# Optimization experiments

Hardware: AMD Instinct MI355X
Metric: run time of the kernel (lower is better)

The kernel has to match this reference:

```python
import jax, jax.numpy as jnp
import numpy as np

D_MODEL = 768
NUM_HEADS = 12
DEPTH = D_MODEL // NUM_HEADS
LN_EPS = 1e-5


def setup_inputs() -> dict:
    key = jax.random.key(0)
    ks = jax.random.split(key, 5)
    B, S = 2, 2048
    scale = 1.0 / np.sqrt(D_MODEL)
    return {
        "Q": jax.random.normal(ks[0], (B, S, D_MODEL), jnp.float32),
        "W_q": jax.random.normal(ks[1], (D_MODEL, D_MODEL), jnp.float32) * scale,
        "b_q": jnp.zeros((D_MODEL,), jnp.float32),
        "W_k": jax.random.normal(ks[2], (D_MODEL, D_MODEL), jnp.float32) * scale,
        "b_k": jnp.zeros((D_MODEL,), jnp.float32),
        "W_v": jax.random.normal(ks[3], (D_MODEL, D_MODEL), jnp.float32) * scale,
        "b_v": jnp.zeros((D_MODEL,), jnp.float32),
        "W_o": jax.random.normal(ks[4], (D_MODEL, D_MODEL), jnp.float32) * scale,
        "b_o": jnp.zeros((D_MODEL,), jnp.float32),
        "ln_gamma": jnp.ones((D_MODEL,), jnp.float32),
        "ln_beta": jnp.zeros((D_MODEL,), jnp.float32),
    }


def _split_heads(x, B):
    # [B, S, D] -> [B, H, S, depth]
    return x.reshape(B, -1, NUM_HEADS, DEPTH).transpose(0, 2, 1, 3)


def reference(Q, W_q, b_q, W_k, b_k, W_v, b_v, W_o, b_o, ln_gamma, ln_beta):
    B = Q.shape[0]
    residual = Q
    # torch Linear: x @ W.T + b
    q = _split_heads(Q @ W_q.T + b_q, B)  # [B,H,S,dh]
    k = _split_heads(Q @ W_k.T + b_k, B)
    v = _split_heads(Q @ W_v.T + b_v, B)
    scores = jnp.einsum("bhqd,bhkd->bhqk", q, k) / jnp.sqrt(jnp.float32(DEPTH))
    attn = jax.nn.softmax(scores, axis=-1)
    out = jnp.einsum("bhqk,bhkd->bhqd", attn, v)
    out = out.transpose(0, 2, 1, 3).reshape(B, -1, D_MODEL)
    out = out @ W_o.T + b_o
    x = out + residual
    mu = jnp.mean(x, axis=-1, keepdims=True)
    var = jnp.mean(jnp.square(x - mu), axis=-1, keepdims=True)
    return (x - mu) * jax.lax.rsqrt(var + LN_EPS) * ln_gamma + ln_beta
```

## Files before the change

kernel.cpp:

```cpp
#include <hip/hip_runtime.h>
#include <hip/hip_bf16.h>

#define D_MODEL 768
#define S_LEN   2048
#define BATCH   2
#define NHEAD   12
#define DH      64
#define NTOK    (BATCH * S_LEN)

typedef __attribute__((ext_vector_type(8))) short bf16x8;
typedef __attribute__((ext_vector_type(4))) float f32x4;

__device__ inline unsigned short f2bf(float f) {
    union { float f; unsigned u; } v; v.f = f;
    unsigned u = v.u;
    u += 0x7fffu + ((u >> 16) & 1u);
    return (unsigned short)(u >> 16);
}

__device__ inline unsigned pack_bf2(float a, float b) {
    union { __hip_bfloat162 h2; unsigned u; } cv;
    cv.h2 = __float22bfloat162_rn(make_float2(a, b));
    return cv.u;
}

__device__ inline void stage16(const void* g, void* l) {
    __builtin_amdgcn_global_load_lds(
        (const __attribute__((address_space(1))) unsigned*)g,
        (__attribute__((address_space(3))) unsigned*)l, 16, 0, 0);
}

__global__ __launch_bounds__(256) void convert_kernel(
    const float* __restrict__ Q,
    const float* __restrict__ Wq, const float* __restrict__ Wk,
    const float* __restrict__ Wv, const float* __restrict__ Wo,
    unsigned short* __restrict__ Xb,
    unsigned short* __restrict__ Wqb, unsigned short* __restrict__ Wkb,
    unsigned short* __restrict__ Wvb, unsigned short* __restrict__ Wob)
{
    const int XV = NTOK * D_MODEL / 4;
    const int WV = D_MODEL * D_MODEL / 4;
    int idx = blockIdx.x * 256 + threadIdx.x;
    if (idx >= XV + 4 * WV) return;

    const float* src; unsigned short* dst; int off;
    if (idx < XV) { src = Q; dst = Xb; off = idx; }
    else {
        int i2 = idx - XV;
        int seg = i2 / WV; off = i2 - seg * WV;
        if      (seg == 0) { src = Wq; dst = Wqb; }
        else if (seg == 1) { src = Wk; dst = Wkb; }
        else if (seg == 2) { src = Wv; dst = Wvb; }
        else               { src = Wo; dst = Wob; }
    }
    float4 v = reinterpret_cast<const float4*>(src)[off];
    uint2 o;
    o.x = pack_bf2(v.x, v.y);
    o.y = pack_bf2(v.z, v.w);
    reinterpret_cast<uint2*>(dst)[off] = o;
}

#define STAGE_TILE(glob, rowstrideB, row0, k0, ldsbase, nIss)                 \
    _Pragma("unroll")                                                          \
    for (int i = 0; i < (nIss); ++i) {                                         \
        int L = i * 4096 + wv * 1024 + lane * 16;                              \
        int row = L >> 7;                                                      \
        int colb = (L & 127) ^ ((row & 7) << 4);                               \
        stage16((const char*)(glob) + (size_t)((row0) + row) * (rowstrideB)    \
                    + ((k0) << 1) + colb,                                      \
                (char*)(ldsbase) + i * 4096 + wv * 1024);                      \
    }

__global__ __launch_bounds__(256) void qkv_gemm_kernel(
    const unsigned short* __restrict__ Xb,
    const unsigned short* __restrict__ Wall,
    const float* __restrict__ bq, const float* __restrict__ bk,
    const float* __restrict__ bv,
    unsigned short* __restrict__ qb, unsigned short* __restrict__ kb,
    unsigned short* __restrict__ vtb)
{
    const int lane = threadIdx.x & 63;
    const int wv   = threadIdx.x >> 6;
    const int lr   = lane & 15;
    const int lg   = lane >> 4;
    const int row0g = blockIdx.y * 128;
    const int col0g = blockIdx.x * 64;

    __shared__ __align__(16) unsigned short At[2][128 * 64];
    __shared__ __align__(16) unsigned short Bt[2][64 * 64];

    f32x4 acc[2][4] = {};

    STAGE_TILE(Xb,   1536, row0g, 0, At[0], 4);
    STAGE_TILE(Wall, 1536, col0g, 0, Bt[0], 2);
    __syncthreads();

    for (int s = 0; s < 12; ++s) {
        int cur = s & 1;
        if (s < 11) {
            STAGE_TILE(Xb,   1536, row0g, (s + 1) * 64, At[cur ^ 1], 4);
            STAGE_TILE(Wall, 1536, col0g, (s + 1) * 64, Bt[cur ^ 1], 2);
        }
        bf16x8 a[2][2], b[4][2];
#pragma unroll
        for (int m = 0; m < 2; ++m) {
            int row = wv * 32 + m * 16 + lr, sw = (row & 7) << 4;
#pragma unroll
            for (int ks = 0; ks < 2; ++ks)
                a[m][ks] = *reinterpret_cast<const bf16x8*>(
                    (const char*)At[cur] + row * 128 + ((ks * 64 + lg * 16) ^ sw));
        }
#pragma unroll
        for (int n = 0; n < 4; ++n) {
            int row = n * 16 + lr, sw = (row & 7) << 4;
#pragma unroll
            for (int ks = 0; ks < 2; ++ks)
                b[n][ks] = *reinterpret_cast<const bf16x8*>(
                    (const char*)Bt[cur] + row * 128 + ((ks * 64 + lg * 16) ^ sw));
        }
#pragma unroll
        for (int ks = 0; ks < 2; ++ks)
#pragma unroll
            for (int m = 0; m < 2; ++m)
#pragma unroll
                for (int n = 0; n < 4; ++n)
                    acc[m][n] = __builtin_amdgcn_mfma_f32_16x16x32_bf16(
                        a[m][ks], b[n][ks], acc[m][n], 0, 0, 0);
        __syncthreads();
    }

    const int which   = blockIdx.x / 12;
    const int colbase = (blockIdx.x % 12) * 64;
    const float* bias = (which == 0) ? bq : (which == 1) ? bk : bv;
#pragma unroll
    for (int m = 0; m < 2; ++m) {
#pragma unroll
        for (int n = 0; n < 4; ++n) {
            int col = colbase + n * 16 + lr;
            float bval = bias[col];
            int h = col >> 6, d = col & 63;
            int rowg = row0g + wv * 32 + m * 16 + lg * 4;
            int bb = rowg >> 11, s0 = rowg & 2047;
            if (which == 2) {
                uint2 w;
                w.x = pack_bf2(acc[m][n][0] + bval, acc[m][n][1] + bval);
                w.y = pack_bf2(acc[m][n][2] + bval, acc[m][n][3] + bval);
                *reinterpret_cast<uint2*>(
                    vtb + ((size_t)(bb * NHEAD + h) * DH + d) * S_LEN + s0) = w;
            } else {
                unsigned short* dst = (which == 0) ? qb : kb;
#pragma unroll
                for (int r = 0; r < 4; ++r)
                    dst[((size_t)(bb * NHEAD + h) * S_LEN + s0 + r) * DH + d] =
                        f2bf(acc[m][n][r] + bval);
            }
        }
    }
}

#define ATTN_CHUNK(P, CI)                                                      \
    {                                                                          \
        if ((CI) < 31) {                                                       \
            stage16(kg0, sdK[(P) ^ 1]);                                        \
            stage16(kg1, sdK[(P) ^ 1] + 4096);                                 \
            stage16(vg0, sdV[(P) ^ 1]);                                        \
            stage16(vg1, sdV[(P) ^ 1] + 4096);                                 \
            kg0 += 8192; kg1 += 8192; vg0 += 128; vg1 += 128;                  \
        }                                                                      \
        f32x4 s[4] = {};                                                       \
        __builtin_amdgcn_s_setprio(1);                                         \
        _Pragma("unroll")                                                      \
        for (int kt = 0; kt < 4; ++kt) {                                       \
            bf16x8 ak0 = *(const bf16x8*)(rdK[P] + kt * 2048);                 \
            bf16x8 ak1 = *(const bf16x8*)(rdK[P] + kt * 2048 + oD);            \
            s[kt] = __builtin_amdgcn_mfma_f32_16x16x32_bf16(ak0, bq0, s[kt], 0, 0, 0); \
            s[kt] = __builtin_amdgcn_mfma_f32_16x16x32_bf16(ak1, bq1, s[kt], 0, 0, 0); \
        }                                                                      \
        __builtin_amdgcn_s_setprio(0);                                         \
        bf16x8 av0[4], av1[4];                                                 \
        _Pragma("unroll")                                                      \
        for (int t = 0; t < 4; ++t) {                                          \
            av0[t] = *(const bf16x8*)(rdV[P] + t * 2048);                      \
            av1[t] = *(const bf16x8*)(rdV[P] + t * 2048 + oD);                 \
        }                                                                      \
        float mxr = fmaxf(fmaxf(fmaxf(s[0][0], s[0][1]), fmaxf(s[0][2], s[0][3])), \
                          fmaxf(fmaxf(s[1][0], s[1][1]), fmaxf(s[1][2], s[1][3]))); \
        mxr = fmaxf(mxr, fmaxf(fmaxf(fmaxf(s[2][0], s[2][1]), fmaxf(s[2][2], s[2][3])), \
                               fmaxf(fmaxf(s[3][0], s[3][1]), fmaxf(s[3][2], s[3][3])))); \
        mxr = fmaxf(mxr, __shfl_xor(mxr, 16));                                 \
        mxr = fmaxf(mxr, __shfl_xor(mxr, 32));                                 \
        float mxs = mxr * SC;                                                  \
        if (__any(mxs > m + 8.0f)) {                                           \
            float mn = fmaxf(m, mxs);                                          \
            float sf = __builtin_amdgcn_exp2f(m - mn);                         \
            m = mn; l *= sf;                                                   \
            _Pragma("unroll")                                                  \
            for (int t = 0; t < 4; ++t) acc[t] *= sf;                          \
        }                                                                      \
        float p[16];                                                           \
        _Pragma("unroll")                                                      \
        for (int kt = 0; kt < 4; ++kt)                                         \
            _Pragma("unroll")                                                  \
            for (int r = 0; r < 4; ++r)                                        \
                p[kt * 4 + r] = __builtin_amdgcn_exp2f(fmaf(s[kt][r], SC, -m)); \
        float sum = ((p[0] + p[1]) + (p[2] + p[3])) + ((p[4] + p[5]) + (p[6] + p[7])); \
        sum += ((p[8] + p[9]) + (p[10] + p[11])) + ((p[12] + p[13]) + (p[14] + p[15])); \
        sum += __shfl_xor(sum, 16);                                            \
        sum += __shfl_xor(sum, 32);                                            \
        l += sum;                                                              \
        _Pragma("unroll")                                                      \
        for (int kt = 0; kt < 4; ++kt) {                                       \
            uint2 w;                                                           \
            w.x = pack_bf2(p[kt * 4 + 0], p[kt * 4 + 1]);                      \
            w.y = pack_bf2(p[kt * 4 + 2], p[kt * 4 + 3]);                      \
            *(uint2*)(plw + ((kt * 32 + lg * 8) ^ swr)) = w;                   \
        }                                                                      \
        union { bf16x8 v; uint2 u[2]; } bp0, bp1;                              \
        bp0.u[0] = *(const uint2*)(plr);                                       \
        bp0.u[1] = *(const uint2*)(plr + 8);                                   \
        bp1.u[0] = *(const uint2*)(plr + oD);                                  \
        bp1.u[1] = *(const uint2*)(plr + oD + 8);                              \
        __builtin_amdgcn_s_setprio(1);                                         \
        _Pragma("unroll")                                                      \
        for (int t = 0; t < 4; ++t) {                                          \
            acc[t] = __builtin_amdgcn_mfma_f32_16x16x32_bf16(av0[t], bp0.v, acc[t], 0, 0, 0); \
            acc[t] = __builtin_amdgcn_mfma_f32_16x16x32_bf16(av1[t], bp1.v, acc[t], 0, 0, 0); \
        }                                                                      \
        __builtin_amdgcn_s_setprio(0);                                         \
        __syncthreads();                                                       \
    }

__global__ __launch_bounds__(256) void attn_kernel(
    const unsigned short* __restrict__ qb, const unsigned short* __restrict__ kb,
    const unsigned short* __restrict__ vtb,
    unsigned short* __restrict__ attnb)
{
    const int lane = threadIdx.x & 63;
    const int wv   = threadIdx.x >> 6;
    const int lr   = lane & 15;
    const int lg   = lane >> 4;
    const int bh   = blockIdx.y;
    const int h    = bh % NHEAD, bb = bh / NHEAD;
    const int q0   = blockIdx.x * 64 + wv * 16;

    __shared__ __align__(16) unsigned short Kt[2][64 * 64];
    __shared__ __align__(16) unsigned short Vt[2][64 * 64];
    __shared__ __align__(16) unsigned short PL[4][16][64];

    const char* kbase = (const char*)(kb  + (size_t)bh * S_LEN * DH);
    const char* vbase = (const char*)(vtb + (size_t)bh * DH * S_LEN);
    const unsigned short* qptr = qb + ((size_t)bh * S_LEN + q0) * DH;

    bf16x8 bq0 = *reinterpret_cast<const bf16x8*>(qptr + (size_t)lr * DH + lg * 8);
    bf16x8 bq1 = *reinterpret_cast<const bf16x8*>(qptr + (size_t)lr * DH + 32 + lg * 8);

    const int swr = (lr & 7) << 4;
    const int o0  = (lg * 16) ^ swr;
    const int oD  = (o0 ^ 64) - o0;
    const int L1  = wv * 1024 + lane * 16;
    const int r1  = L1 >> 7;
    const int cb1 = (L1 & 127) ^ ((r1 & 7) << 4);

    const char* kg0 = kbase + (size_t)r1 * 128 + cb1;
    const char* kg1 = kbase + (size_t)(32 + r1) * 128 + cb1;
    const char* vg0 = vbase + (size_t)r1 * 4096 + cb1;
    const char* vg1 = vbase + (size_t)(32 + r1) * 4096 + cb1;

    char* sdK[2] = { (char*)Kt[0] + wv * 1024, (char*)Kt[1] + wv * 1024 };
    char* sdV[2] = { (char*)Vt[0] + wv * 1024, (char*)Vt[1] + wv * 1024 };
    const char* rdK[2] = {
        (const char*)Kt[0] + lr * 128 + o0,
        (const char*)Kt[1] + lr * 128 + o0 };
    const char* rdV[2] = {
        (const char*)Vt[0] + lr * 128 + o0,
        (const char*)Vt[1] + lr * 128 + o0 };
    char* plw = (char*)PL + wv * 2048 + lr * 128;
    const char* plr = plw + o0;

    float m = -1e30f, l = 0.f;
    f32x4 acc[4] = {};
    const float SC = 0.125f * 1.44269504088896f;

    stage16(kg0, sdK[0]); stage16(kg1, sdK[0] + 4096);
    stage16(vg0, sdV[0]); stage16(vg1, sdV[0] + 4096);
    kg0 += 8192; kg1 += 8192; vg0 += 128; vg1 += 128;
    __syncthreads();

    for (int it = 0; it < 16; ++it) {
        ATTN_CHUNK(0, it * 2);
        ATTN_CHUNK(1, it * 2 + 1);
    }

    float rl = 1.0f / l;
    size_t rowbase = ((size_t)(bb * S_LEN + q0 + lr)) * D_MODEL + h * DH;
#pragma unroll
    for (int t = 0; t < 4; ++t) {
        unsigned w0 = pack_bf2(acc[t][0] * rl, acc[t][1] * rl);
        unsigned w1 = pack_bf2(acc[t][2] * rl, acc[t][3] * rl);
        *reinterpret_cast<unsigned*>(attnb + rowbase + t * 16 + lg * 4)     = w0;
        *reinterpret_cast<unsigned*>(attnb + rowbase + t * 16 + lg * 4 + 2) = w1;
    }
}

__global__ __launch_bounds__(256) void oproj_kernel(
    const unsigned short* __restrict__ attnb, const unsigned short* __restrict__ Wob,
    const float* __restrict__ bo, const float* __restrict__ Qres,
    float* __restrict__ Y)
{
    const int lane = threadIdx.x & 63;
    const int wv   = threadIdx.x >> 6;
    const int lr   = lane & 15;
    const int lg   = lane >> 4;
    const int row0g = blockIdx.y * 128;
    const int col0g = blockIdx.x * 64;

    __shared__ __align__(16) unsigned short At[2][128 * 64];
    __shared__ __align__(16) unsigned short Bt[2][64 * 64];

    f32x4 acc[2][4] = {};

    STAGE_TILE(attnb, 1536, row0g, 0, At[0], 4);
    STAGE_TILE(Wob,   1536, col0g, 0, Bt[0], 2);
    __syncthreads();

    for (int s = 0; s < 12; ++s) {
        int cur = s & 1;
        if (s < 11) {
            STAGE_TILE(attnb, 1536, row0g, (s + 1) * 64, At[cur ^ 1], 4);
            STAGE_TILE(Wob,   1536, col0g, (s + 1) * 64, Bt[cur ^ 1], 2);
        }
        bf16x8 a[2][2], b[4][2];
#pragma unroll
        for (int m = 0; m < 2; ++m) {
            int row = wv * 32 + m * 16 + lr, sw = (row & 7) << 4;
#pragma unroll
            for (int ks = 0; ks < 2; ++ks)
                a[m][ks] = *reinterpret_cast<const bf16x8*>(
                    (const char*)At[cur] + row * 128 + ((ks * 64 + lg * 16) ^ sw));
        }
#pragma unroll
        for (int n = 0; n < 4; ++n) {
            int row = n * 16 + lr, sw = (row & 7) << 4;
#pragma unroll
            for (int ks = 0; ks < 2; ++ks)
                b[n][ks] = *reinterpret_cast<const bf16x8*>(
                    (const char*)Bt[cur] + row * 128 + ((ks * 64 + lg * 16) ^ sw));
        }
#pragma unroll
        for (int ks = 0; ks < 2; ++ks)
#pragma unroll
            for (int m = 0; m < 2; ++m)
#pragma unroll
                for (int n = 0; n < 4; ++n)
                    acc[m][n] = __builtin_amdgcn_mfma_f32_16x16x32_bf16(
                        a[m][ks], b[n][ks], acc[m][n], 0, 0, 0);
        __syncthreads();
    }

#pragma unroll
    for (int m = 0; m < 2; ++m)
#pragma unroll
        for (int n = 0; n < 4; ++n) {
            int col = col0g + n * 16 + lr;
            float bval = bo[col];
#pragma unroll
            for (int r = 0; r < 4; ++r) {
                int row = row0g + wv * 32 + m * 16 + lg * 4 + r;
                size_t off = (size_t)row * D_MODEL + col;
                Y[off] = acc[m][n][r] + bval + Qres[off];
            }
        }
}

__global__ __launch_bounds__(256) void ln_kernel(
    const float* __restrict__ Y,
    const float* __restrict__ gamma, const float* __restrict__ beta,
    float* __restrict__ out)
{
    const int lane = threadIdx.x & 63;
    const int row  = blockIdx.x * 4 + (threadIdx.x >> 6);
    const float4* yr = reinterpret_cast<const float4*>(Y + (size_t)row * D_MODEL);

    float4 v[3];
    float sum = 0.f, ss = 0.f;
#pragma unroll
    for (int j = 0; j < 3; ++j) {
        v[j] = yr[lane + 64 * j];
        sum += v[j].x + v[j].y + v[j].z + v[j].w;
        ss  += v[j].x * v[j].x + v[j].y * v[j].y + v[j].z * v[j].z + v[j].w * v[j].w;
    }
#pragma unroll
    for (int msk = 1; msk < 64; msk <<= 1) {
        sum += __shfl_xor(sum, msk);
        ss  += __shfl_xor(ss,  msk);
    }
    float mu  = sum * (1.f / 768.f);
    float var = ss * (1.f / 768.f) - mu * mu;
    float is  = rsqrtf(var + 1e-5f);

    const float4* g4 = reinterpret_cast<const float4*>(gamma);
    const float4* b4 = reinterpret_cast<const float4*>(beta);
    float4* o4 = reinterpret_cast<float4*>(out + (size_t)row * D_MODEL);
#pragma unroll
    for (int j = 0; j < 3; ++j) {
        float4 g = g4[lane + 64 * j], b = b4[lane + 64 * j], r;
        r.x = (v[j].x - mu) * is * g.x + b.x;
        r.y = (v[j].y - mu) * is * g.y + b.y;
        r.z = (v[j].z - mu) * is * g.z + b.z;
        r.w = (v[j].w - mu) * is * g.w + b.w;
        o4[lane + 64 * j] = r;
    }
}

extern "C" void kernel_launch(void* const* d_in, const int* in_sizes, int n_in,
                              void* d_out, int out_size, void* d_ws, size_t ws_size,
                              hipStream_t stream)
{
    const float* Q     = (const float*)d_in[0];
    const float* Wq    = (const float*)d_in[1];
    const float* bq    = (const float*)d_in[2];
    const float* Wk    = (const float*)d_in[3];
    const float* bk    = (const float*)d_in[4];
    const float* Wv    = (const float*)d_in[5];
    const float* bv    = (const float*)d_in[6];
    const float* Wo    = (const float*)d_in[7];
    const float* bo    = (const float*)d_in[8];
    const float* gamma = (const float*)d_in[9];
    const float* beta  = (const float*)d_in[10];
    float* out = (float*)d_out;

    char* ws = (char*)d_ws;
    unsigned short* Xb    = (unsigned short*)(ws + 0);
    unsigned short* Wqb   = (unsigned short*)(ws + 6291456);
    unsigned short* Wkb   = (unsigned short*)(ws + 7471104);
    unsigned short* Wvb   = (unsigned short*)(ws + 8650752);
    unsigned short* Wob   = (unsigned short*)(ws + 9830400);
    unsigned short* qb    = (unsigned short*)(ws + 11010048);
    unsigned short* kb    = (unsigned short*)(ws + 17301504);
    unsigned short* vtb   = (unsigned short*)(ws + 23592960);
    unsigned short* attnb = (unsigned short*)(ws + 29884416);
    float*          Yf    = (float*)        (ws + 36175872);

    convert_kernel<<<5376, 256, 0, stream>>>(Q, Wq, Wk, Wv, Wo, Xb, Wqb, Wkb, Wvb, Wob);
    qkv_gemm_kernel<<<dim3(36, 32), 256, 0, stream>>>(Xb, Wqb, bq, bk, bv, qb, kb, vtb);
    attn_kernel<<<dim3(32, 24), 256, 0, stream>>>(qb, kb, vtb, attnb);
    oproj_kernel<<<dim3(12, 32), 256, 0, stream>>>(attnb, Wob, bo, Q, Yf);
    ln_kernel<<<1024, 256, 0, stream>>>(Yf, gamma, beta, out);
}
```

Before: 110.9 us.

## Split attention over key halves with 8-wave blocks and a combine pass

```diff
diff --git a/kernel.cpp b/kernel.cpp
--- a/kernel.cpp
+++ b/kernel.cpp
@@ -7,6 +7,7 @@
 #define NHEAD   12
 #define DH      64
 #define NTOK    (BATCH * S_LEN)
+#define NBH     (BATCH * NHEAD)
 
 typedef __attribute__((ext_vector_type(8))) short bf16x8;
 typedef __attribute__((ext_vector_type(4))) float f32x4;
@@ -22,6 +23,10 @@
     union { __hip_bfloat162 h2; unsigned u; } cv;
     cv.h2 = __float22bfloat162_rn(make_float2(a, b));
     return cv.u;
+}
+
+__device__ inline float bf2f(unsigned short u) {
+    union { unsigned u; float f; } c; c.u = ((unsigned)u) << 16; return c.f;
 }
 
 __device__ inline void stage16(const void* g, void* l) {
@@ -158,14 +163,15 @@
     }
 }
 
-#define ATTN_CHUNK(P, CI)                                                      \
+#define ATTN_CHUNK(P, CI, NCHUNK)                                              \
     {                                                                          \
-        if ((CI) < 31) {                                                       \
-            stage16(kg0, sdK[(P) ^ 1]);                                        \
-            stage16(kg1, sdK[(P) ^ 1] + 4096);                                 \
-            stage16(vg0, sdV[(P) ^ 1]);                                        \
-            stage16(vg1, sdV[(P) ^ 1] + 4096);                                 \
-            kg0 += 8192; kg1 += 8192; vg0 += 128; vg1 += 128;                  \
+        if ((CI) < (NCHUNK) - 1) {                                             \
+            _Pragma("unroll")                                                  \
+            for (int i = 0; i < SPW; ++i) {                                    \
+                stage16(kg[i], sdK[(P) ^ 1] + i * 1024);                       \
+                stage16(vg[i], sdV[(P) ^ 1] + i * 1024);                       \
+                kg[i] += 8192; vg[i] += 128;                                   \
+            }                                                                  \
         }                                                                      \
         f32x4 s[4] = {};                                                       \
         __builtin_amdgcn_s_setprio(1);                                         \
@@ -213,13 +219,13 @@
             uint2 w;                                                           \
             w.x = pack_bf2(p[kt * 4 + 0], p[kt * 4 + 1]);                      \
             w.y = pack_bf2(p[kt * 4 + 2], p[kt * 4 + 3]);                      \
-            *(uint2*)(plw + ((kt * 32 + lg * 8) ^ swr)) = w;                   \
+            *(uint2*)(plw + kt * 32 + lg * 8) = w;                             \
         }                                                                      \
         union { bf16x8 v; uint2 u[2]; } bp0, bp1;                              \
         bp0.u[0] = *(const uint2*)(plr);                                       \
         bp0.u[1] = *(const uint2*)(plr + 8);                                   \
-        bp1.u[0] = *(const uint2*)(plr + oD);                                  \
-        bp1.u[1] = *(const uint2*)(plr + oD + 8);                              \
+        bp1.u[0] = *(const uint2*)(plr + 64);                                  \
+        bp1.u[1] = *(const uint2*)(plr + 72);                                  \
         __builtin_amdgcn_s_setprio(1);                                         \
         _Pragma("unroll")                                                      \
         for (int t = 0; t < 4; ++t) {                                          \
@@ -230,25 +236,34 @@
         __syncthreads();                                                       \
     }
 
-__global__ __launch_bounds__(256) void attn_kernel(
+template<int NW, int KS>
+__global__ __launch_bounds__(NW * 64) void attn_kernel(
     const unsigned short* __restrict__ qb, const unsigned short* __restrict__ kb,
     const unsigned short* __restrict__ vtb,
-    unsigned short* __restrict__ attnb)
-{
+    unsigned short* __restrict__ attnb,
+    unsigned short* __restrict__ Opart,
+    float2* __restrict__ mlbuf)
+{
+    constexpr int SPW    = 8192 / (NW * 1024);
+    constexpr int NCHUNK = 32 / KS;
+
     const int lane = threadIdx.x & 63;
     const int wv   = threadIdx.x >> 6;
     const int lr   = lane & 15;
     const int lg   = lane >> 4;
     const int bh   = blockIdx.y;
     const int h    = bh % NHEAD, bb = bh / NHEAD;
-    const int q0   = blockIdx.x * 64 + wv * 16;
-
-    __shared__ __align__(16) unsigned short Kt[2][64 * 64];
-    __shared__ __align__(16) unsigned short Vt[2][64 * 64];
-    __shared__ __align__(16) unsigned short PL[4][16][64];
-
-    const char* kbase = (const char*)(kb  + (size_t)bh * S_LEN * DH);
-    const char* vbase = (const char*)(vtb + (size_t)bh * DH * S_LEN);
+    const int q0   = blockIdx.x * (NW * 16) + wv * 16;
+    const int ks   = (KS == 2) ? blockIdx.z : 0;
+
+    __shared__ __align__(16) unsigned short Kt[2][4096];
+    __shared__ __align__(16) unsigned short Vt[2][4096];
+    __shared__ __align__(16) unsigned short PL[NW][16][68];
+
+    const char* kbase = (const char*)(kb  + (size_t)bh * S_LEN * DH)
+                        + (size_t)ks * (S_LEN / KS) * 128;
+    const char* vbase = (const char*)(vtb + (size_t)bh * DH * S_LEN)
+                        + (size_t)ks * (S_LEN / KS) * 2;
     const unsigned short* qptr = qb + ((size_t)bh * S_LEN + q0) * DH;
 
     bf16x8 bq0 = *reinterpret_cast<const bf16x8*>(qptr + (size_t)lr * DH + lg * 8);
@@ -257,49 +272,100 @@
     const int swr = (lr & 7) << 4;
     const int o0  = (lg * 16) ^ swr;
     const int oD  = (o0 ^ 64) - o0;
-    const int L1  = wv * 1024 + lane * 16;
-    const int r1  = L1 >> 7;
-    const int cb1 = (L1 & 127) ^ ((r1 & 7) << 4);
-
-    const char* kg0 = kbase + (size_t)r1 * 128 + cb1;
-    const char* kg1 = kbase + (size_t)(32 + r1) * 128 + cb1;
-    const char* vg0 = vbase + (size_t)r1 * 4096 + cb1;
-    const char* vg1 = vbase + (size_t)(32 + r1) * 4096 + cb1;
-
-    char* sdK[2] = { (char*)Kt[0] + wv * 1024, (char*)Kt[1] + wv * 1024 };
-    char* sdV[2] = { (char*)Vt[0] + wv * 1024, (char*)Vt[1] + wv * 1024 };
+
+    const char* kg[SPW];
+    const char* vg[SPW];
+#pragma unroll
+    for (int i = 0; i < SPW; ++i) {
+        int L = wv * SPW * 1024 + i * 1024 + lane * 16;
+        int r = L >> 7;
+        int c = (L & 127) ^ ((r & 7) << 4);
+        kg[i] = kbase + (size_t)r * 128 + c;
+        vg[i] = vbase + (size_t)r * 4096 + c;
+    }
+    char* sdK[2] = { (char*)Kt[0] + wv * SPW * 1024, (char*)Kt[1] + wv * SPW * 1024 };
+    char* sdV[2] = { (char*)Vt[0] + wv * SPW * 1024, (char*)Vt[1] + wv * SPW * 1024 };
     const char* rdK[2] = {
         (const char*)Kt[0] + lr * 128 + o0,
         (const char*)Kt[1] + lr * 128 + o0 };
     const char* rdV[2] = {
         (const char*)Vt[0] + lr * 128 + o0,
         (const char*)Vt[1] + lr * 128 + o0 };
-    char* plw = (char*)PL + wv * 2048 + lr * 128;
-    const char* plr = plw + o0;
+    char* plw = (char*)PL + wv * 2176 + lr * 136;
+    const char* plr = plw + lg * 16;
 
     float m = -1e30f, l = 0.f;
     f32x4 acc[4] = {};
     const float SC = 0.125f * 1.44269504088896f;
 
-    stage16(kg0, sdK[0]); stage16(kg1, sdK[0] + 4096);
-    stage16(vg0, sdV[0]); stage16(vg1, sdV[0] + 4096);
-    kg0 += 8192; kg1 += 8192; vg0 += 128; vg1 += 128;
+#pragma unroll
+    for (int i = 0; i < SPW; ++i) {
+        stage16(kg[i], sdK[0] + i * 1024);
+        stage16(vg[i], sdV[0] + i * 1024);
+        kg[i] += 8192; vg[i] += 128;
+    }
     __syncthreads();
 
-    for (int it = 0; it < 16; ++it) {
-        ATTN_CHUNK(0, it * 2);
-        ATTN_CHUNK(1, it * 2 + 1);
-    }
-
-    float rl = 1.0f / l;
-    size_t rowbase = ((size_t)(bb * S_LEN + q0 + lr)) * D_MODEL + h * DH;
-#pragma unroll
-    for (int t = 0; t < 4; ++t) {
-        unsigned w0 = pack_bf2(acc[t][0] * rl, acc[t][1] * rl);
-        unsigned w1 = pack_bf2(acc[t][2] * rl, acc[t][3] * rl);
-        *reinterpret_cast<unsigned*>(attnb + rowbase + t * 16 + lg * 4)     = w0;
-        *reinterpret_cast<unsigned*>(attnb + rowbase + t * 16 + lg * 4 + 2) = w1;
-    }
+    for (int it = 0; it < NCHUNK / 2; ++it) {
+        ATTN_CHUNK(0, it * 2, NCHUNK);
+        ATTN_CHUNK(1, it * 2 + 1, NCHUNK);
+    }
+
+    if constexpr (KS == 1) {
+        float rl = 1.0f / l;
+        size_t rowbase = ((size_t)(bb * S_LEN + q0 + lr)) * D_MODEL + h * DH;
+#pragma unroll
+        for (int t = 0; t < 4; ++t) {
+            unsigned w0 = pack_bf2(acc[t][0] * rl, acc[t][1] * rl);
+            unsigned w1 = pack_bf2(acc[t][2] * rl, acc[t][3] * rl);
+            *reinterpret_cast<unsigned*>(attnb + rowbase + t * 16 + lg * 4)     = w0;
+            *reinterpret_cast<unsigned*>(attnb + rowbase + t * 16 + lg * 4 + 2) = w1;
+        }
+    } else {
+        size_t base = ((size_t)(ks * NBH + bh) * S_LEN + q0 + lr) * 64;
+#pragma unroll
+        for (int t = 0; t < 4; ++t) {
+            unsigned w0 = pack_bf2(acc[t][0], acc[t][1]);
+            unsigned w1 = pack_bf2(acc[t][2], acc[t][3]);
+            *reinterpret_cast<unsigned*>(Opart + base + t * 16 + lg * 4)     = w0;
+            *reinterpret_cast<unsigned*>(Opart + base + t * 16 + lg * 4 + 2) = w1;
+        }
+        if (lg == 0)
+            mlbuf[(size_t)(ks * NBH + bh) * S_LEN + q0 + lr] = make_float2(m, l);
+    }
+}
+
+__global__ __launch_bounds__(256) void combine_kernel(
+    const unsigned short* __restrict__ Opart,
+    const float2* __restrict__ mlbuf,
+    unsigned short* __restrict__ attnb)
+{
+    int idx = blockIdx.x * 256 + threadIdx.x;
+    int d4  = idx & 15;
+    int h   = (idx >> 4) % 12;
+    int tok = idx / 192;
+    int bb  = tok >> 11, s = tok & 2047;
+    size_t qoff = (size_t)(bb * NHEAD + h) * S_LEN + s;
+
+    float2 ml0 = mlbuf[qoff];
+    float2 ml1 = mlbuf[(size_t)NBH * S_LEN + qoff];
+    float M  = fmaxf(ml0.x, ml1.x);
+    float w0 = __builtin_amdgcn_exp2f(ml0.x - M);
+    float w1 = __builtin_amdgcn_exp2f(ml1.x - M);
+    float ri = 1.0f / (w0 * ml0.y + w1 * ml1.y);
+    w0 *= ri; w1 *= ri;
+
+    size_t ob = qoff * 64 + d4 * 4;
+    ushort4 a = *reinterpret_cast<const ushort4*>(Opart + ob);
+    ushort4 b = *reinterpret_cast<const ushort4*>(Opart + (size_t)NBH * S_LEN * 64 + ob);
+    float o0 = bf2f(a.x) * w0 + bf2f(b.x) * w1;
+    float o1 = bf2f(a.y) * w0 + bf2f(b.y) * w1;
+    float o2 = bf2f(a.z) * w0 + bf2f(b.z) * w1;
+    float o3 = bf2f(a.w) * w0 + bf2f(b.w) * w1;
+    uint2 w;
+    w.x = pack_bf2(o0, o1);
+    w.y = pack_bf2(o2, o3);
+    *reinterpret_cast<uint2*>(attnb + (size_t)tok * D_MODEL + h * 64 + d4 * 4) = w;
 }
 
 __global__ __launch_bounds__(256) void oproj_kernel(
@@ -440,10 +506,21 @@
     unsigned short* vtb   = (unsigned short*)(ws + 23592960);
     unsigned short* attnb = (unsigned short*)(ws + 29884416);
     float*          Yf    = (float*)        (ws + 36175872);
+    unsigned short* Opartb = (unsigned short*)(ws + 36175872);
+    float2*         mlbuf  = (float2*)       (ws + 61341696);
+
+    const bool splitk = (ws_size >= 62128128ull);
 
     convert_kernel<<<5376, 256, 0, stream>>>(Q, Wq, Wk, Wv, Wo, Xb, Wqb, Wkb, Wvb, Wob);
     qkv_gemm_kernel<<<dim3(36, 32), 256, 0, stream>>>(Xb, Wqb, bq, bk, bv, qb, kb, vtb);
-    attn_kernel<<<dim3(32, 24), 256, 0, stream>>>(qb, kb, vtb, attnb);
+    if (splitk) {
+        attn_kernel<8, 2><<<dim3(16, 24, 2), 512, 0, stream>>>(qb, kb, vtb, attnb,
+                                                               Opartb, mlbuf);
+        combine_kernel<<<3072, 256, 0, stream>>>(Opartb, mlbuf, attnb);
+    } else {
+        attn_kernel<4, 1><<<dim3(32, 24), 256, 0, stream>>>(qb, kb, vtb, attnb,
+                                                            Opartb, mlbuf);
+    }
     oproj_kernel<<<dim3(12, 32), 256, 0, stream>>>(attnb, Wob, bo, Q, Yf);
     ln_kernel<<<1024, 256, 0, stream>>>(Yf, gamma, beta, out);
 }
```

Result: no change. 111.4 us (+0.4%).
